# Kernel optimization log

Hardware: AMD Instinct MI355X
Metric: run time of the kernel (lower is better)

Reference implementation:

```python
import jax, jax.numpy as jnp
import numpy as np

HIDDEN = 1024
HEADS = 16
HEAD_DIM = 64
EPS = 0.001  # numerical_stabilizer


def setup_inputs() -> dict:
    key = jax.random.key(0)
    kq, kk, kv, kwq, kwk, kwv = jax.random.split(key, 6)
    B, S = 4, 4096
    shape = (B, S, HIDDEN)
    # glorot_uniform over (hidden, heads*head_dim) fan
    init = jax.nn.initializers.glorot_uniform()
    wshape = (HIDDEN, HEADS, HEAD_DIM)
    return {
        "query": jax.random.normal(kq, shape, jnp.float32),
        "key": jax.random.normal(kk, shape, jnp.float32),
        "value": jax.random.normal(kv, shape, jnp.float32),
        "query_kernel": init(kwq, wshape, jnp.float32),
        "key_kernel": init(kwk, wshape, jnp.float32),
        "value_kernel": init(kwv, wshape, jnp.float32),
    }


def reference(query, key, value, query_kernel, key_kernel, value_kernel):
    # project: [b,s,d] x [d,n,h] -> [b,s,n,h]
    q = jnp.einsum('bsd,dnh->bsnh', query, query_kernel)
    k = jnp.einsum('bsd,dnh->bsnh', key, key_kernel)
    v = jnp.einsum('bsd,dnh->bsnh', value, value_kernel)
    # relu feature map + stabilizer
    q = jax.nn.relu(q) + EPS
    k = jax.nn.relu(k) + EPS
    # kv aggregation: [b,n,h_k,h_v]
    kvs = jnp.einsum('bsnm,bsnd->bnmd', k, v)
    a_v = jnp.einsum('bsnm,bnmd->bsnd', q, kvs)
    ks_sum = jnp.sum(k, axis=1)                 # [b,n,m]
    normalizer = jnp.einsum('bsnm,bnm->bsn', q, ks_sum)
    a_v = a_v / normalizer[..., None]
    B, S, N, H = a_v.shape
    return a_v.reshape(B, S, N * H)
```

## Files before the change

kernel.cpp:

```cpp
#include <hip/hip_runtime.h>
#include <hip/hip_bf16.h>
#include <cstdint>
#include <cstddef>

#define HIDDEN 1024
#define NHEADS 16
#define HD     64
#define BATCH  4
#define SEQ    4096
#define MTOT   (BATCH*SEQ)
#define EPSF   1e-3f

typedef unsigned short u16;
typedef unsigned int   u32;
typedef __bf16 bf16x8 __attribute__((ext_vector_type(8)));
typedef u16    u16x8  __attribute__((ext_vector_type(8)));
typedef float  f32x4  __attribute__((ext_vector_type(4)));
typedef u32    u32x4  __attribute__((ext_vector_type(4)));

__device__ inline u16 f2bf(float a) {
    __bf16 h = (__bf16)a;
    return __builtin_bit_cast(u16, h);
}
__device__ inline u32 pack2bf(float a, float b) {
    return (u32)f2bf(a) | ((u32)f2bf(b) << 16);
}
__device__ inline float bf2f(u16 x) {
    return __builtin_bit_cast(float, (u32)x << 16);
}
__device__ inline f32x4 mfma16(bf16x8 a, bf16x8 b, f32x4 c) {
    return __builtin_amdgcn_mfma_f32_16x16x32_bf16(a, b, c, 0, 0, 0);
}
__device__ inline void gl_lds16(const void* g, void* l) {
    __builtin_amdgcn_global_load_lds(
        (const __attribute__((address_space(1))) void*)g,
        (__attribute__((address_space(3))) void*)l,
        16, 0, 0);
}

__global__ __launch_bounds__(256) void prep_kernel(
    const float* __restrict__ W0, const float* __restrict__ W1,
    const float* __restrict__ W2, u16* __restrict__ Wt,
    float* __restrict__ zero_base)
{
    const int t = threadIdx.x;
    if (blockIdx.z == 3) {
        const int base = (blockIdx.y * 16 + blockIdx.x) * 256 + t;
        const int total = 64*64*64 + 64*64;
        for (int idx = base; idx < total; idx += 65536) zero_base[idx] = 0.f;
        return;
    }
    const int z = blockIdx.z;
    const float* __restrict__ W = (z == 0) ? W0 : ((z == 1) ? W1 : W2);
    u16* __restrict__ Wz = Wt + (size_t)z * HIDDEN * HIDDEN;
    const int d0 = blockIdx.y * 64, c0 = blockIdx.x * 64;
    __shared__ u16 T[64 * 72];
    {
        const int r = t & 63, p = t >> 6;
        const float* src = W + (size_t)(d0 + r) * HIDDEN + c0 + p * 16;
        f32x4 x0 = *(const f32x4*)src,       x1 = *(const f32x4*)(src + 4);
        f32x4 x2 = *(const f32x4*)(src + 8), x3 = *(const f32x4*)(src + 12);
        u32x4 y0 = { pack2bf(x0[0],x0[1]), pack2bf(x0[2],x0[3]),
                     pack2bf(x1[0],x1[1]), pack2bf(x1[2],x1[3]) };
        u32x4 y1 = { pack2bf(x2[0],x2[1]), pack2bf(x2[2],x2[3]),
                     pack2bf(x3[0],x3[1]), pack2bf(x3[2],x3[3]) };
        *(u32x4*)((char*)T + (size_t)(r * 72 + p * 16) * 2)     = y0;
        *(u32x4*)((char*)T + (size_t)(r * 72 + p * 16 + 8) * 2) = y1;
    }
    __syncthreads();
    {
        const int c = t & 63, p = t >> 6;
        u16 vals[16];
        #pragma unroll
        for (int i = 0; i < 16; ++i) vals[i] = T[(p * 16 + i) * 72 + c];
        u16* dst = Wz + (size_t)(c0 + c) * HIDDEN + d0 + p * 16;
        *(u16x8*)dst       = *(const u16x8*)&vals[0];
        *(u16x8*)(dst + 8) = *(const u16x8*)&vals[8];
    }
}

__global__ __launch_bounds__(256) void gemm_proj(
    const float* __restrict__ X0, const float* __restrict__ X1,
    const float* __restrict__ X2, const u16* __restrict__ Wt,
    u16* __restrict__ P)
{
    const int z = blockIdx.z;
    const float* __restrict__ X = (z == 0) ? X0 : ((z == 1) ? X1 : X2);
    const u16* __restrict__ W = Wt + (size_t)z * HIDDEN * HIDDEN;
    u16* __restrict__ Pz = P + (size_t)z * ((size_t)MTOT * HIDDEN);
    const int doact = (z < 2);

    const int lin = blockIdx.y * 8 + blockIdx.x;
    const int swz = (lin & 7) * 128 + (lin >> 3);
    const int m0 = (swz >> 3) * 128;
    const int n0 = (swz & 7) * 128;

    __shared__ u16 As[128 * 64];
    __shared__ u16 Bs[128 * 64];

    const int t = threadIdx.x, lane = t & 63, wid = t >> 6;
    const int wr = (wid >> 1) * 64, wc = (wid & 1) * 64;
    const int l15 = lane & 15, l4 = lane >> 4;
    const int arow = t >> 3, acol = t & 7;
    const int brow = lane >> 3;
    const int bchunk = (lane & 7) ^ brow;

    f32x4 acc[4][4];
    #pragma unroll
    for (int i = 0; i < 4; ++i)
        #pragma unroll
        for (int j = 0; j < 4; ++j) acc[i][j] = f32x4{0.f, 0.f, 0.f, 0.f};

    f32x4 a0[4], a1[4];
    #pragma unroll
    for (int i = 0; i < 4; ++i) {
        const float* ap = X + (size_t)(m0 + arow + 32 * i) * HIDDEN + acol * 8;
        a0[i] = *(const f32x4*)ap;
        a1[i] = *(const f32x4*)(ap + 4);
    }

    for (int kt = 0; kt < HIDDEN / 64; ++kt) {
        const int k0 = kt * 64;
        __syncthreads();
        #pragma unroll
        for (int i = 0; i < 4; ++i) {
            const int r = arow + 32 * i;
            const int cd = acol ^ (r & 7);
            u32x4 apk = { pack2bf(a0[i][0], a0[i][1]), pack2bf(a0[i][2], a0[i][3]),
                          pack2bf(a1[i][0], a1[i][1]), pack2bf(a1[i][2], a1[i][3]) };
            *(u32x4*)((char*)As + (size_t)r * 128 + cd * 16) = apk;
        }
        #pragma unroll
        for (int g = 0; g < 4; ++g) {
            const int rbase = wid * 32 + g * 8;
            gl_lds16(W + (size_t)(n0 + rbase + brow) * HIDDEN + k0 + bchunk * 8,
                     &Bs[rbase * 64]);
        }
        if (kt + 1 < HIDDEN / 64) {
            #pragma unroll
            for (int i = 0; i < 4; ++i) {
                const float* ap = X + (size_t)(m0 + arow + 32 * i) * HIDDEN
                                    + (k0 + 64) + acol * 8;
                a0[i] = *(const f32x4*)ap;
                a1[i] = *(const f32x4*)(ap + 4);
            }
        }
        __syncthreads();
        #pragma unroll
        for (int ks = 0; ks < 2; ++ks) {
            bf16x8 af[4], bfr[4];
            #pragma unroll
            for (int mi = 0; mi < 4; ++mi) {
                const int r = wr + mi * 16 + l15;
                const int c = (ks * 4 + l4) ^ (r & 7);
                af[mi] = *(const bf16x8*)((const char*)As + (size_t)r * 128 + c * 16);
            }
            #pragma unroll
            for (int ni = 0; ni < 4; ++ni) {
                const int r = wc + ni * 16 + l15;
                const int c = (ks * 4 + l4) ^ (r & 7);
                bfr[ni] = *(const bf16x8*)((const char*)Bs + (size_t)r * 128 + c * 16);
            }
            #pragma unroll
            for (int mi = 0; mi < 4; ++mi)
                #pragma unroll
                for (int ni = 0; ni < 4; ++ni)
                    acc[mi][ni] = mfma16(af[mi], bfr[ni], acc[mi][ni]);
        }
    }
    #pragma unroll
    for (int mi = 0; mi < 4; ++mi) {
        #pragma unroll
        for (int ni = 0; ni < 4; ++ni) {
            const int mrow = m0 + wr + mi * 16 + l4 * 4;
            const int ncol = n0 + wc + ni * 16 + l15;
            #pragma unroll
            for (int r = 0; r < 4; ++r) {
                float v = acc[mi][ni][r];
                if (doact) v = fmaxf(v, 0.f) + EPSF;
                Pz[(size_t)(mrow + r) * HIDDEN + ncol] = f2bf(v);
            }
        }
    }
}

__global__ __launch_bounds__(256) void kvs_kernel(
    const u16* __restrict__ Kp, const u16* __restrict__ Vp,
    float* __restrict__ kvsT, float* __restrict__ ks_sum)
{
    const int bn = blockIdx.x, sc = blockIdx.y;
    const int b = bn >> 4, n = bn & 15;
    __shared__ float Ks[64 * 64];
    __shared__ float Vs[64 * 64];
    const int t = threadIdx.x;
    const int tm = t & 15, td = t >> 4;
    float acc[4][4] = {};
    float ksa[4] = {0.f, 0.f, 0.f, 0.f};
    const size_t rowbase = ((size_t)b * SEQ + (size_t)sc * 256) * HIDDEN + n * 64;

    for (int st = 0; st < 4; ++st) {
        __syncthreads();
        #pragma unroll
        for (int i = 0; i < 2; ++i) {
            const int j = i * 256 + t;
            const int r = j >> 3, c = j & 7;
            const size_t off = rowbase + (size_t)(st * 64 + r) * HIDDEN + c * 8;
            u16x8 kk = *(const u16x8*)(Kp + off);
            u16x8 vv = *(const u16x8*)(Vp + off);
            f32x4 ka{bf2f(kk[0]), bf2f(kk[1]), bf2f(kk[2]), bf2f(kk[3])};
            f32x4 kb{bf2f(kk[4]), bf2f(kk[5]), bf2f(kk[6]), bf2f(kk[7])};
            f32x4 va{bf2f(vv[0]), bf2f(vv[1]), bf2f(vv[2]), bf2f(vv[3])};
            f32x4 vb{bf2f(vv[4]), bf2f(vv[5]), bf2f(vv[6]), bf2f(vv[7])};
            *(f32x4*)&Ks[r * 64 + c * 8]     = ka;
            *(f32x4*)&Ks[r * 64 + c * 8 + 4] = kb;
            *(f32x4*)&Vs[r * 64 + c * 8]     = va;
            *(f32x4*)&Vs[r * 64 + c * 8 + 4] = vb;
        }
        __syncthreads();
        for (int s = 0; s < 64; ++s) {
            const f32x4 kk = *(const f32x4*)&Ks[s * 64 + tm * 4];
            const f32x4 vv = *(const f32x4*)&Vs[s * 64 + td * 4];
            #pragma unroll
            for (int i = 0; i < 4; ++i) {
                ksa[i] += kk[i];
                #pragma unroll
                for (int j = 0; j < 4; ++j) acc[i][j] += kk[i] * vv[j];
            }
        }
    }
    float* kt_bn = kvsT + (size_t)bn * 64 * 64;
    #pragma unroll
    for (int j = 0; j < 4; ++j)
        #pragma unroll
        for (int i = 0; i < 4; ++i)
            atomicAdd(&kt_bn[(td * 4 + j) * 64 + tm * 4 + i], acc[i][j]);
    if (td == 0) {
        #pragma unroll
        for (int i = 0; i < 4; ++i)
            atomicAdd(&ks_sum[bn * 64 + tm * 4 + i], ksa[i]);
    }
}

__global__ __launch_bounds__(256) void out_kernel(
    const u16* __restrict__ Qp, const float* __restrict__ kvsT,
    const float* __restrict__ ks_sum, float* __restrict__ out)
{
    const int bn = blockIdx.x, sc = blockIdx.y;
    const int b = bn >> 4, n = bn & 15;
    __shared__ u16 Aq[256 * 64];
    __shared__ u16 Bk[64 * 64];
    __shared__ float ksl[64];
    __shared__ float nrm[256];
    const int t = threadIdx.x, lane = t & 63, wid = t >> 6;
    const int l15 = lane & 15, l4 = lane >> 4;
    const size_t qbase = ((size_t)b * SEQ + (size_t)sc * 256) * HIDDEN + n * 64;

    #pragma unroll
    for (int i = 0; i < 8; ++i) {
        const int j = i * 256 + t;
        const int r = j >> 3, c = j & 7;
        u16x8 q8 = *(const u16x8*)(Qp + qbase + (size_t)r * HIDDEN + c * 8);
        *(u16x8*)((char*)Aq + (size_t)r * 128 + ((c ^ (r & 7)) * 16)) = q8;
    }
    {
        const int d = t & 63, p = t >> 6;
        const float* src = kvsT + ((size_t)bn * 64 + d) * 64 + p * 16;
        f32x4 x0 = *(const f32x4*)src,        x1 = *(const f32x4*)(src + 4);
        f32x4 x2 = *(const f32x4*)(src + 8),  x3 = *(const f32x4*)(src + 12);
        u32x4 y0 = { pack2bf(x0[0],x0[1]), pack2bf(x0[2],x0[3]),
                     pack2bf(x1[0],x1[1]), pack2bf(x1[2],x1[3]) };
        u32x4 y1 = { pack2bf(x2[0],x2[1]), pack2bf(x2[2],x2[3]),
                     pack2bf(x3[0],x3[1]), pack2bf(x3[2],x3[3]) };
        *(u32x4*)((char*)Bk + (size_t)d * 128 + (((p * 2)     ^ (d & 7)) * 16)) = y0;
        *(u32x4*)((char*)Bk + (size_t)d * 128 + (((p * 2 + 1) ^ (d & 7)) * 16)) = y1;
    }
    if (t < 16) ((f32x4*)ksl)[t] = ((const f32x4*)(ks_sum + bn * 64))[t];
    __syncthreads();
    {
        float s = 0.f;
        #pragma unroll
        for (int c = 0; c < 8; ++c) {
            u16x8 q8 = *(const u16x8*)((const char*)Aq + (size_t)t * 128 + ((c ^ (t & 7)) * 16));
            #pragma unroll
            for (int e = 0; e < 8; ++e) s += bf2f(q8[e]) * ksl[c * 8 + e];
        }
        nrm[t] = s;
    }
    __syncthreads();
    f32x4 acc[4][4];
    #pragma unroll
    for (int i = 0; i < 4; ++i)
        #pragma unroll
        for (int j = 0; j < 4; ++j) acc[i][j] = f32x4{0.f, 0.f, 0.f, 0.f};
    #pragma unroll
    for (int ks = 0; ks < 2; ++ks) {
        bf16x8 af[4], bfr[4];
        #pragma unroll
        for (int mi = 0; mi < 4; ++mi) {
            const int r = wid * 64 + mi * 16 + l15;
            const int c = (ks * 4 + l4) ^ (r & 7);
            af[mi] = *(const bf16x8*)((const char*)Aq + (size_t)r * 128 + c * 16);
        }
        #pragma unroll
        for (int ni = 0; ni < 4; ++ni) {
            const int rd = ni * 16 + l15;
            const int c = (ks * 4 + l4) ^ (rd & 7);
            bfr[ni] = *(const bf16x8*)((const char*)Bk + (size_t)rd * 128 + c * 16);
        }
        #pragma unroll
        for (int mi = 0; mi < 4; ++mi)
            #pragma unroll
            for (int ni = 0; ni < 4; ++ni)
                acc[mi][ni] = mfma16(af[mi], bfr[ni], acc[mi][ni]);
    }
    const size_t obase = (size_t)b * SEQ + (size_t)sc * 256;
    #pragma unroll
    for (int mi = 0; mi < 4; ++mi) {
        const int s0l = wid * 64 + mi * 16 + l4 * 4;
        const float rn0 = 1.f / nrm[s0l],     rn1 = 1.f / nrm[s0l + 1];
        const float rn2 = 1.f / nrm[s0l + 2], rn3 = 1.f / nrm[s0l + 3];
        #pragma unroll
        for (int ni = 0; ni < 4; ++ni) {
            const int d = ni * 16 + l15;
            float* op = out + (obase + s0l) * (size_t)HIDDEN + n * 64 + d;
            op[0 * HIDDEN] = acc[mi][ni][0] * rn0;
            op[1 * HIDDEN] = acc[mi][ni][1] * rn1;
            op[2 * HIDDEN] = acc[mi][ni][2] * rn2;
            op[3 * HIDDEN] = acc[mi][ni][3] * rn3;
        }
    }
}

extern "C" void kernel_launch(void* const* d_in, const int* in_sizes, int n_in,
                              void* d_out, int out_size, void* d_ws, size_t ws_size,
                              hipStream_t stream)
{
    const float* Xq = (const float*)d_in[0];
    const float* Xk = (const float*)d_in[1];
    const float* Xv = (const float*)d_in[2];
    const float* Wq = (const float*)d_in[3];
    const float* Wk = (const float*)d_in[4];
    const float* Wv = (const float*)d_in[5];
    float* out = (float*)d_out;

    char* w = (char*)d_ws;
    u16*   Wt   = (u16*)w;
    u16*   P    = (u16*)(w + 6291456);
    u16*   Pq   = P;
    u16*   Pk   = P + (size_t)MTOT * HIDDEN;
    u16*   Pv   = P + 2 * (size_t)MTOT * HIDDEN;
    float* kvsT = (float*)(w + 6291456 + 3 * 33554432);
    float* ks   = (float*)(w + 6291456 + 3 * 33554432 + 1048576);

    prep_kernel<<<dim3(16, 16, 4), 256, 0, stream>>>(Wq, Wk, Wv, Wt, kvsT);
    gemm_proj<<<dim3(8, 128, 3), 256, 0, stream>>>(Xq, Xk, Xv, Wt, P);
    kvs_kernel<<<dim3(64, 16), 256, 0, stream>>>(Pk, Pv, kvsT, ks);
    out_kernel<<<dim3(64, 16), 256, 0, stream>>>(Pq, kvsT, ks, out);
}
```

Before: 465.2 us.

## Double-buffer LDS tiles in projection GEMM and halve kvs grid

The projection GEMM gets two LDS buffers for A and B. The next tile is written and staged while MFMAs run on the current one, the A prefetch moves two k-steps ahead, and only one barrier is kept per iteration. This is meant to hide global-to-LDS latency and cut a barrier, at the cost of doubled LDS use (64KB per block), which may lower occupancy. The kvs kernel now covers 512 sequence rows per block with half as many blocks, which halves the atomic or partial reductions but gives less parallelism.

```diff
diff --git a/kernel.cpp b/kernel.cpp
--- a/kernel.cpp
+++ b/kernel.cpp
@@ -95,8 +95,8 @@
     const int m0 = (swz >> 3) * 128;
     const int n0 = (swz & 7) * 128;
 
-    __shared__ u16 As[128 * 64];
-    __shared__ u16 Bs[128 * 64];
+    __shared__ u16 As[2][128 * 64];
+    __shared__ u16 Bs[2][128 * 64];
 
     const int t = threadIdx.x, lane = t & 63, wid = t >> 6;
     const int wr = (wid >> 1) * 64, wc = (wid & 1) * 64;
@@ -112,40 +112,54 @@
         for (int j = 0; j < 4; ++j) acc[i][j] = f32x4{0.f, 0.f, 0.f, 0.f};
 
     f32x4 a0[4], a1[4];
-    #pragma unroll
-    for (int i = 0; i < 4; ++i) {
-        const float* ap = X + (size_t)(m0 + arow + 32 * i) * HIDDEN + acol * 8;
-        a0[i] = *(const f32x4*)ap;
-        a1[i] = *(const f32x4*)(ap + 4);
-    }
-
-    for (int kt = 0; kt < HIDDEN / 64; ++kt) {
-        const int k0 = kt * 64;
-        __syncthreads();
-        #pragma unroll
-        for (int i = 0; i < 4; ++i) {
-            const int r = arow + 32 * i;
-            const int cd = acol ^ (r & 7);
-            u32x4 apk = { pack2bf(a0[i][0], a0[i][1]), pack2bf(a0[i][2], a0[i][3]),
-                          pack2bf(a1[i][0], a1[i][1]), pack2bf(a1[i][2], a1[i][3]) };
-            *(u32x4*)((char*)As + (size_t)r * 128 + cd * 16) = apk;
-        }
-        #pragma unroll
-        for (int g = 0; g < 4; ++g) {
-            const int rbase = wid * 32 + g * 8;
-            gl_lds16(W + (size_t)(n0 + rbase + brow) * HIDDEN + k0 + bchunk * 8,
-                     &Bs[rbase * 64]);
-        }
-        if (kt + 1 < HIDDEN / 64) {
-            #pragma unroll
-            for (int i = 0; i < 4; ++i) {
-                const float* ap = X + (size_t)(m0 + arow + 32 * i) * HIDDEN
-                                    + (k0 + 64) + acol * 8;
-                a0[i] = *(const f32x4*)ap;
-                a1[i] = *(const f32x4*)(ap + 4);
-            }
-        }
-        __syncthreads();
+
+#define LOAD_A(KT)                                                           \
+    {                                                                        \
+        _Pragma("unroll")                                                    \
+        for (int i = 0; i < 4; ++i) {                                        \
+            const float* ap = X + (size_t)(m0 + arow + 32 * i) * HIDDEN      \
+                                + (KT) * 64 + acol * 8;                      \
+            a0[i] = *(const f32x4*)ap;                                       \
+            a1[i] = *(const f32x4*)(ap + 4);                                 \
+        }                                                                    \
+    }
+#define WRITE_A(BUF)                                                         \
+    {                                                                        \
+        _Pragma("unroll")                                                    \
+        for (int i = 0; i < 4; ++i) {                                        \
+            const int r = arow + 32 * i;                                     \
+            const int cd = acol ^ (r & 7);                                   \
+            u32x4 apk = { pack2bf(a0[i][0], a0[i][1]),                       \
+                          pack2bf(a0[i][2], a0[i][3]),                       \
+                          pack2bf(a1[i][0], a1[i][1]),                       \
+                          pack2bf(a1[i][2], a1[i][3]) };                     \
+            *(u32x4*)((char*)As[BUF] + (size_t)r * 128 + cd * 16) = apk;     \
+        }                                                                    \
+    }
+#define STAGE_B(BUF, KT)                                                     \
+    {                                                                        \
+        _Pragma("unroll")                                                    \
+        for (int g = 0; g < 4; ++g) {                                        \
+            const int rbase = wid * 32 + g * 8;                              \
+            gl_lds16(W + (size_t)(n0 + rbase + brow) * HIDDEN                \
+                       + (KT) * 64 + bchunk * 8,                             \
+                     &Bs[BUF][rbase * 64]);                                  \
+        }                                                                    \
+    }
+
+    LOAD_A(0);
+    WRITE_A(0);
+    STAGE_B(0, 0);
+    LOAD_A(1);
+    __syncthreads();
+
+    for (int kt = 0; kt < 16; ++kt) {
+        const int cur = kt & 1;
+        if (kt + 1 < 16) {
+            WRITE_A(cur ^ 1);
+            STAGE_B(cur ^ 1, kt + 1);
+        }
+        if (kt + 2 < 16) LOAD_A(kt + 2);
         #pragma unroll
         for (int ks = 0; ks < 2; ++ks) {
             bf16x8 af[4], bfr[4];
@@ -153,13 +167,13 @@
             for (int mi = 0; mi < 4; ++mi) {
                 const int r = wr + mi * 16 + l15;
                 const int c = (ks * 4 + l4) ^ (r & 7);
-                af[mi] = *(const bf16x8*)((const char*)As + (size_t)r * 128 + c * 16);
+                af[mi] = *(const bf16x8*)((const char*)As[cur] + (size_t)r * 128 + c * 16);
             }
             #pragma unroll
             for (int ni = 0; ni < 4; ++ni) {
                 const int r = wc + ni * 16 + l15;
                 const int c = (ks * 4 + l4) ^ (r & 7);
-                bfr[ni] = *(const bf16x8*)((const char*)Bs + (size_t)r * 128 + c * 16);
+                bfr[ni] = *(const bf16x8*)((const char*)Bs[cur] + (size_t)r * 128 + c * 16);
             }
             #pragma unroll
             for (int mi = 0; mi < 4; ++mi)
@@ -167,7 +181,12 @@
                 for (int ni = 0; ni < 4; ++ni)
                     acc[mi][ni] = mfma16(af[mi], bfr[ni], acc[mi][ni]);
         }
-    }
+        __syncthreads();
+    }
+#undef LOAD_A
+#undef WRITE_A
+#undef STAGE_B
+
     #pragma unroll
     for (int mi = 0; mi < 4; ++mi) {
         #pragma unroll
@@ -196,9 +215,9 @@
     const int tm = t & 15, td = t >> 4;
     float acc[4][4] = {};
     float ksa[4] = {0.f, 0.f, 0.f, 0.f};
-    const size_t rowbase = ((size_t)b * SEQ + (size_t)sc * 256) * HIDDEN + n * 64;
-
-    for (int st = 0; st < 4; ++st) {
+    const size_t rowbase = ((size_t)b * SEQ + (size_t)sc * 512) * HIDDEN + n * 64;
+
+    for (int st = 0; st < 8; ++st) {
         __syncthreads();
         #pragma unroll
         for (int i = 0; i < 2; ++i) {
@@ -354,6 +373,6 @@
 
     prep_kernel<<<dim3(16, 16, 4), 256, 0, stream>>>(Wq, Wk, Wv, Wt, kvsT);
     gemm_proj<<<dim3(8, 128, 3), 256, 0, stream>>>(Xq, Xk, Xv, Wt, P);
-    kvs_kernel<<<dim3(64, 16), 256, 0, stream>>>(Pk, Pv, kvsT, ks);
+    kvs_kernel<<<dim3(64, 8), 256, 0, stream>>>(Pk, Pv, kvsT, ks);
     out_kernel<<<dim3(64, 16), 256, 0, stream>>>(Pq, kvsT, ks, out);
 }
```

Result: faster. 442.6 us (-4.8%).
